# Optimization experiments

Measured on AMD Instinct MI355X. Metric: run time of the kernel, lower is better.

The kernel has to match this reference:

```python
import jax, jax.numpy as jnp
import numpy as np

M_CHANNELS = 256
N_KNOTS = 64
EPS = 1e-6


def setup_inputs() -> dict:
    key = jax.random.key(0)
    k_u, k_c = jax.random.split(key)
    u = jax.random.uniform(k_u, (4096, 64, M_CHANNELS), dtype=jnp.float32)
    # knots: per-channel sorted ascending, init linspace(0,1) as in the module
    knots = jnp.tile(jnp.linspace(0.0, 1.0, N_KNOTS, dtype=jnp.float32)[None, :],
                     (M_CHANNELS, 1))
    # coefs init to zeros in the module; use randn for a non-degenerate test
    coefs = jax.random.normal(k_c, (M_CHANNELS, N_KNOTS), dtype=jnp.float32)
    return {"u": u, "knots": knots, "coefs": coefs}


def reference(u, knots, coefs):
    """Piecewise-linear spline eval, vectorized over channels and points.
    u: [..., M], knots/coefs: [M, K] (knots sorted ascending per channel).
    """
    m, K = knots.shape
    orig_shape = u.shape
    flat = u.reshape(-1, m).T  # [M, N]
    # torch.bucketize(right=False) == searchsorted side='left'
    idx = jax.vmap(lambda k, x: jnp.searchsorted(k, x, side='left'))(knots, flat)
    idx0 = jnp.clip(idx - 1, 0, K - 2)  # [M, N]
    idx1 = idx0 + 1
    k0 = jnp.take_along_axis(knots, idx0, axis=1)
    k1 = jnp.take_along_axis(knots, idx1, axis=1)
    c0 = jnp.take_along_axis(coefs, idx0, axis=1)
    c1 = jnp.take_along_axis(coefs, idx1, axis=1)
    t = (flat - k0) / (k1 - k0 + EPS)
    out = c0 + t * (c1 - c0)  # [M, N]
    return out.T.reshape(orig_shape)
```

## Files before the change

kernel.cpp:

```cpp
#include <hip/hip_runtime.h>


#define EPS 1e-6f
#define NCH_GROUP 32
#define NGROUPS 8
#define BLOCKS_PER_GROUP 128
#define ROWS_PER_TILE 32

typedef float f32x4 __attribute__((ext_vector_type(4)));

__global__ __launch_bounds__(256) void bspline_kernel(
    const float* __restrict__ u, const float* __restrict__ knots,
    const float* __restrict__ coefs, float* __restrict__ out, int n_rows)
{
    __shared__ f32x4 sP[NCH_GROUP * 64];

    const int t = threadIdx.x;
    const int g = blockIdx.x & (NGROUPS - 1);
    const int b = blockIdx.x >> 3;

    const float* gk = knots + (size_t)g * NCH_GROUP * 64;
    const float* gc = coefs + (size_t)g * NCH_GROUP * 64;
    for (int i = t; i < NCH_GROUP * 63; i += 256) {
        int c = i / 63;
        int j = i - c * 63;
        f32x4 p;
        p.x = gk[c * 64 + j];
        p.y = gk[c * 64 + j + 1];
        p.z = gc[c * 64 + j];
        p.w = gc[c * 64 + j + 1];
        sP[(c << 6) + j] = p;
    }
    __syncthreads();

    const int col4 = t & 7;
    const int rsub = t >> 3;
    const int lc = col4 * 4;

    float kmin[4], scale[4];
#pragma unroll
    for (int cc = 0; cc < 4; ++cc) {
        float klo = sP[(lc + cc) << 6].x;
        float khi = sP[((lc + cc) << 6) + 62].y;
        kmin[cc] = klo;
        scale[cc] = 63.0f * __builtin_amdgcn_rcpf(khi - klo);
    }

    const f32x4* u4 = (const f32x4*)u;
    f32x4* o4 = (f32x4*)out;
    const int colbase = g * 8 + col4;
    const int ntiles = n_rows / ROWS_PER_TILE;

    for (int rt = b; rt < ntiles; rt += BLOCKS_PER_GROUP) {
        int row = rt * ROWS_PER_TILE + rsub;
        size_t idx = (size_t)row * 64 + colbase;
        f32x4 x4 = u4[idx];
        f32x4 r;
#pragma unroll
        for (int cc = 0; cc < 4; ++cc) {
            float x = x4[cc];
            const f32x4* pc = &sP[(lc + cc) << 6];

            float xs = (x - kmin[cc]) * scale[cc];
            int j = (int)xs;
            j = max(0, min(62, j));
            f32x4 p = pc[j];
            while (j > 0 && p.x >= x) { --j; p = pc[j]; }
            while (j < 62 && p.y < x) { ++j; p = pc[j]; }

            float tt = (x - p.x) * __builtin_amdgcn_rcpf(p.y - p.x + EPS);
            r[cc] = fmaf(tt, p.w - p.z, p.z);
        }
        o4[idx] = r;
    }
}

extern "C" void kernel_launch(void* const* d_in, const int* in_sizes, int n_in,
                              void* d_out, int out_size, void* d_ws, size_t ws_size,
                              hipStream_t stream) {
    const float* u     = (const float*)d_in[0];
    const float* knots = (const float*)d_in[1];
    const float* coefs = (const float*)d_in[2];
    float* out = (float*)d_out;

    int n_rows = in_sizes[0] / 256;

    dim3 grid(NGROUPS * BLOCKS_PER_GROUP);
    dim3 block(256);
    bspline_kernel<<<grid, block, 0, stream>>>(u, knots, coefs, out, n_rows);
}
```

Before: 450.2 us.

## Split knot/coef LDS tables with XOR swizzle and widen channel groups

```diff
diff --git a/kernel.cpp b/kernel.cpp
--- a/kernel.cpp
+++ b/kernel.cpp
@@ -2,53 +2,56 @@
 
 
 #define EPS 1e-6f
-#define NCH_GROUP 32
-#define NGROUPS 8
-#define BLOCKS_PER_GROUP 128
-#define ROWS_PER_TILE 32
+#define NCH_GROUP 128
+#define NGROUPS 2
+#define BLOCKS_PER_GROUP 256
+#define ROWS_PER_TILE 16
 
 typedef float f32x4 __attribute__((ext_vector_type(4)));
 
-__global__ __launch_bounds__(256) void bspline_kernel(
+__global__ __launch_bounds__(512) void bspline_kernel(
     const float* __restrict__ u, const float* __restrict__ knots,
     const float* __restrict__ coefs, float* __restrict__ out, int n_rows)
 {
-    __shared__ f32x4 sP[NCH_GROUP * 64];
+    __shared__ float sK[NCH_GROUP * 64];
+    __shared__ float sC[NCH_GROUP * 64];
 
     const int t = threadIdx.x;
     const int g = blockIdx.x & (NGROUPS - 1);
-    const int b = blockIdx.x >> 3;
+    const int b = blockIdx.x >> 1;
 
     const float* gk = knots + (size_t)g * NCH_GROUP * 64;
     const float* gc = coefs + (size_t)g * NCH_GROUP * 64;
-    for (int i = t; i < NCH_GROUP * 63; i += 256) {
-        int c = i / 63;
-        int j = i - c * 63;
-        f32x4 p;
-        p.x = gk[c * 64 + j];
-        p.y = gk[c * 64 + j + 1];
-        p.z = gc[c * 64 + j];
-        p.w = gc[c * 64 + j + 1];
-        sP[(c << 6) + j] = p;
+    for (int i = t; i < NCH_GROUP * 64; i += 512) {
+        int c = i >> 6;
+        int j = i & 63;
+        int s = (c << 6) | (j ^ (c & 31));
+        sK[s] = gk[i];
+        sC[s] = gc[i];
     }
     __syncthreads();
 
-    const int col4 = t & 7;
-    const int rsub = t >> 3;
+    const int col4 = t & 31;
+    const int rsub = t >> 5;
     const int lc = col4 * 4;
 
     float kmin[4], scale[4];
+    int xm[4];
 #pragma unroll
     for (int cc = 0; cc < 4; ++cc) {
-        float klo = sP[(lc + cc) << 6].x;
-        float khi = sP[((lc + cc) << 6) + 62].y;
+        int c = lc + cc;
+        int m = c & 31;
+        xm[cc] = m;
+        const float* kp = &sK[c << 6];
+        float klo = kp[0 ^ m];
+        float khi = kp[63 ^ m];
         kmin[cc] = klo;
         scale[cc] = 63.0f * __builtin_amdgcn_rcpf(khi - klo);
     }
 
     const f32x4* u4 = (const f32x4*)u;
     f32x4* o4 = (f32x4*)out;
-    const int colbase = g * 8 + col4;
+    const int colbase = g * 32 + col4;
     const int ntiles = n_rows / ROWS_PER_TILE;
 
     for (int rt = b; rt < ntiles; rt += BLOCKS_PER_GROUP) {
@@ -59,17 +62,22 @@
 #pragma unroll
         for (int cc = 0; cc < 4; ++cc) {
             float x = x4[cc];
-            const f32x4* pc = &sP[(lc + cc) << 6];
+            const int m = xm[cc];
+            const float* kp = &sK[(lc + cc) << 6];
+            const float* cp = &sC[(lc + cc) << 6];
 
             float xs = (x - kmin[cc]) * scale[cc];
             int j = (int)xs;
             j = max(0, min(62, j));
-            f32x4 p = pc[j];
-            while (j > 0 && p.x >= x) { --j; p = pc[j]; }
-            while (j < 62 && p.y < x) { ++j; p = pc[j]; }
+            float k0 = kp[j ^ m];
+            float k1 = kp[(j + 1) ^ m];
+            while (j > 0 && k0 >= x) { --j; k1 = k0; k0 = kp[j ^ m]; }
+            while (j < 62 && k1 < x) { ++j; k0 = k1; k1 = kp[(j + 1) ^ m]; }
 
-            float tt = (x - p.x) * __builtin_amdgcn_rcpf(p.y - p.x + EPS);
-            r[cc] = fmaf(tt, p.w - p.z, p.z);
+            float tt = (x - k0) * __builtin_amdgcn_rcpf(k1 - k0 + EPS);
+            float c0 = cp[j ^ m];
+            float c1 = cp[(j + 1) ^ m];
+            r[cc] = fmaf(tt, c1 - c0, c0);
         }
         o4[idx] = r;
     }
@@ -86,6 +94,6 @@
     int n_rows = in_sizes[0] / 256;
 
     dim3 grid(NGROUPS * BLOCKS_PER_GROUP);
-    dim3 block(256);
+    dim3 block(512);
     bspline_kernel<<<grid, block, 0, stream>>>(u, knots, coefs, out, n_rows);
 }
```

Result: faster. 435.5 us (-3.3%).
